# Optimization experiments

Measured on AMD Instinct MI355X. Metric: run time of the kernel, lower is better.

## Reference

```python
import jax, jax.numpy as jnp
import numpy as np

N = 100000   # nodes
E = 1600000  # edges
G = 64       # graphs
D_IN, D_H, D_OUT = 128, 128, 64


def setup_inputs() -> dict:
    key = jax.random.key(0)
    ks = jax.random.split(key, 24)
    def p(k, shape, fan_in):
        return jax.random.normal(k, shape, jnp.float32) / np.sqrt(fan_in)
    inp = {
        "x": jax.random.normal(ks[0], (N, D_IN), jnp.float32),
        "W0r": p(ks[1], (D_H, D_IN), D_IN), "W0i": p(ks[2], (D_H, D_IN), D_IN),
        "b0r": jnp.zeros((D_H,), jnp.float32), "b0i": jnp.zeros((D_H,), jnp.float32),
        "M0r": p(ks[3], (D_H, D_H), D_H), "M0i": p(ks[4], (D_H, D_H), D_H),
        "c0r": jnp.zeros((D_H,), jnp.float32), "c0i": jnp.zeros((D_H,), jnp.float32),
        "t0r": jnp.float32(1.0), "t0i": jnp.zeros((1,), jnp.float32),
        "W1r": p(ks[5], (D_OUT, D_H), D_H), "W1i": p(ks[6], (D_OUT, D_H), D_H),
        "b1r": jnp.zeros((D_OUT,), jnp.float32), "b1i": jnp.zeros((D_OUT,), jnp.float32),
        "M1r": p(ks[7], (D_OUT, D_OUT), D_OUT), "M1i": p(ks[8], (D_OUT, D_OUT), D_OUT),
        "c1r": jnp.zeros((D_OUT,), jnp.float32), "c1i": jnp.zeros((D_OUT,), jnp.float32),
        "t1r": jnp.float32(1.0), "t1i": jnp.zeros((1,), jnp.float32),
        "edge_index": jax.random.randint(ks[9], (2, E), 0, N, dtype=jnp.int64),
        "batch": jnp.sort(jax.random.randint(ks[10], (N,), 0, G, dtype=jnp.int64)),
    }
    return inp


def _complex_relu(z):
    return jax.nn.relu(z.real) + 1j * jax.nn.relu(z.imag)


def _layer(x, Wr, Wi, br, bi, Mr, Mi, cr, ci, tr, ti, src, dst):
    # complex linear: x @ W^T + b
    W = Wr + 1j * Wi
    x = x @ W.T + (br + 1j * bi)
    x = _complex_relu(x)
    t = tr + 1j * ti  # complex time param, shape [1]
    time_factor = jnp.exp(-1j * t)
    # msg_lin applied at node level (linear commutes with gather), then gather at src
    m = (x @ (Mr + 1j * Mi).T + (cr + 1j * ci)) * time_factor
    aggr = jax.ops.segment_sum(m[src], dst, num_segments=N)
    ef = jnp.exp(-1j * t * 0.5)
    return x * ef + aggr * (1 - ef)


def reference(x, W0r, W0i, b0r, b0i, M0r, M0i, c0r, c0i, t0r, t0i,
              W1r, W1i, b1r, b1i, M1r, M1i, c1r, c1i, t1r, t1i,
              edge_index, batch):
    src, dst = edge_index[0], edge_index[1]
    xc = x.astype(jnp.complex64)
    xc = _layer(xc, W0r, W0i, b0r, b0i, M0r, M0i, c0r, c0i, t0r, t0i, src, dst)
    xc = _layer(xc, W1r, W1i, b1r, b1i, M1r, M1i, c1r, c1i, t1r, t1i, src, dst)
    a = jnp.abs(xc)  # [N, D_OUT] float32
    sums = jax.ops.segment_sum(a, batch, num_segments=G)
    counts = jax.ops.segment_sum(jnp.ones((N,), a.dtype), batch, num_segments=G)
    mean = sums / jnp.clip(counts, 1.0)[:, None]
    return jax.nn.log_softmax(mean, axis=1)
```

## Files before the change

kernel.cpp:

```cpp
#include <hip/hip_runtime.h>

typedef __attribute__((ext_vector_type(8))) short bf16x8;
typedef __attribute__((ext_vector_type(4))) float f32x4;

__device__ __forceinline__ float b2f(unsigned short u) {
    return __uint_as_float(((unsigned int)u) << 16);
}
__device__ __forceinline__ unsigned short f2b(float f) {
    unsigned int u = __float_as_uint(f);
    unsigned int r = (u + 0x7FFFu + ((u >> 16) & 1u)) >> 16;
    return (unsigned short)r;
}

__global__ __launch_bounds__(256) void prep_v_cplx_kernel(
    const float* __restrict__ Wr, const float* __restrict__ Wi,
    unsigned short* __restrict__ V, int J, int K)
{
    int idx = blockIdx.x * 256 + threadIdx.x;
    if (idx >= J * K) return;
    int j = idx / K, kk = idx % K;
    float wr = Wr[idx], wi = Wi[idx];
    int Kr = 2 * K;
    unsigned short* r0 = V + (size_t)(2 * j) * Kr + 2 * kk;
    unsigned short* r1 = V + (size_t)(2 * j + 1) * Kr + 2 * kk;
    r0[0] = f2b(wr);  r0[1] = f2b(-wi);
    r1[0] = f2b(wi);  r1[1] = f2b(wr);
}

__global__ __launch_bounds__(256) void prep_v_real_kernel(
    const float* __restrict__ Wr, const float* __restrict__ Wi,
    unsigned short* __restrict__ V, int J, int K)
{
    int idx = blockIdx.x * 256 + threadIdx.x;
    if (idx >= J * K) return;
    int j = idx / K, k = idx % K;
    V[(size_t)(2 * j) * K + k]     = f2b(Wr[idx]);
    V[(size_t)(2 * j + 1) * K + k] = f2b(Wi[idx]);
}

template<int Kr, int TWOJ, bool REAL_IN, bool CRELU, bool MIX, bool WF8>
__global__ __launch_bounds__(256) void mfma_cgemm_kernel(
    const void* __restrict__ Xv,
    const unsigned short* __restrict__ Vg,
    const float* __restrict__ br, const float* __restrict__ bi,
    const float* __restrict__ trp, const float* __restrict__ tip,
    const unsigned short* __restrict__ Hin, const int* __restrict__ degp,
    unsigned short* __restrict__ Out, unsigned char* __restrict__ Of8,
    int nNodes)
{
    constexpr int TILES  = TWOJ / 16;
    constexpr int FT     = TILES / 4;
    constexpr int CHUNKS = Kr / 32;
    constexpr int VROW   = 40;
    static_assert(TILES % 4 == 0, "TILES % 4");

    __shared__ __align__(16) unsigned short sV[TWOJ * VROW];
    __shared__ __align__(16) unsigned short sA[64 * VROW];

    const int tid  = threadIdx.x;
    const int w    = tid >> 6;
    const int lane = tid & 63;
    const int l15  = lane & 15;
    const int q    = lane >> 4;
    const int n0   = blockIdx.x * 64;
    const int tq   = w * FT;

    f32x4 acc[FT][4];
    #pragma unroll
    for (int t = 0; t < FT; ++t)
        #pragma unroll
        for (int nt = 0; nt < 4; ++nt) acc[t][nt] = (f32x4){0.f, 0.f, 0.f, 0.f};

    for (int kc = 0; kc < CHUNKS; ++kc) {
        #pragma unroll
        for (int it = 0; it < TWOJ / 64; ++it) {
            int idx = it * 256 + tid;
            int row = idx >> 2;
            int seg = idx & 3;
            *(uint4*)(sV + row * VROW + seg * 8) =
                *(const uint4*)(Vg + (size_t)row * Kr + kc * 32 + seg * 8);
        }
        if constexpr (REAL_IN) {
            const float* X = (const float*)Xv;
            #pragma unroll
            for (int it = 0; it < 2; ++it) {
                int idx = it * 256 + tid;
                int nl = idx >> 3;
                int cg = idx & 7;
                int n  = n0 + nl;
                float4 v = make_float4(0.f, 0.f, 0.f, 0.f);
                if (n < nNodes)
                    v = *(const float4*)(X + (size_t)n * Kr + kc * 32 + cg * 4);
                *(ushort4*)(sA + nl * VROW + cg * 4) =
                    make_ushort4(f2b(v.x), f2b(v.y), f2b(v.z), f2b(v.w));
            }
        } else {
            const unsigned short* X = (const unsigned short*)Xv;
            int nl  = tid >> 2;
            int seg = tid & 3;
            int n   = n0 + nl;
            uint4 v = make_uint4(0, 0, 0, 0);
            if (n < nNodes)
                v = *(const uint4*)(X + (size_t)n * Kr + kc * 32 + seg * 8);
            *(uint4*)(sA + nl * VROW + seg * 8) = v;
        }
        __syncthreads();

        bf16x8 bfrag[4];
        #pragma unroll
        for (int nt = 0; nt < 4; ++nt)
            bfrag[nt] = *(const bf16x8*)(sA + (nt * 16 + l15) * VROW + q * 8);
        #pragma unroll
        for (int t = 0; t < FT; ++t) {
            bf16x8 afrag = *(const bf16x8*)(sV + ((tq + t) * 16 + l15) * VROW + q * 8);
            #pragma unroll
            for (int nt = 0; nt < 4; ++nt)
                acc[t][nt] = __builtin_amdgcn_mfma_f32_16x16x32_bf16(
                    afrag, bfrag[nt], acc[t][nt], 0, 0, 0);
        }
        __syncthreads();
    }

    float Fr = 1.f, Fi = 0.f, efr = 1.f, efi = 0.f;
    if constexpr (MIX) {
        float tr = trp[0], ti = tip[0];
        float er  = expf(ti);
        float tfr =  er * cosf(tr);
        float tfi = -er * sinf(tr);
        float eh  = expf(0.5f * ti);
        efr =  eh * cosf(0.5f * tr);
        efi = -eh * sinf(0.5f * tr);
        float omr = 1.f - efr, omi = -efi;
        Fr = tfr * omr - tfi * omi;
        Fi = tfr * omi + tfi * omr;
    }
    #pragma unroll
    for (int nt = 0; nt < 4; ++nt) {
        int n = n0 + nt * 16 + l15;
        if (n >= nNodes) continue;
        float dg = 0.f;
        if constexpr (MIX) dg = (float)degp[n];
        #pragma unroll
        for (int t = 0; t < FT; ++t) {
            int f0 = (tq + t) * 16 + q * 4;
            int j0 = f0 >> 1;
            float re0, im0, re1, im1;
            if constexpr (MIX) {
                float ar0 = acc[t][nt][0] + dg * br[j0];
                float ai0 = acc[t][nt][1] + dg * bi[j0];
                float ar1 = acc[t][nt][2] + dg * br[j0 + 1];
                float ai1 = acc[t][nt][3] + dg * bi[j0 + 1];
                re0 = ar0 * Fr - ai0 * Fi;  im0 = ar0 * Fi + ai0 * Fr;
                re1 = ar1 * Fr - ai1 * Fi;  im1 = ar1 * Fi + ai1 * Fr;
                ushort4 hu = *(const ushort4*)(Hin + (size_t)n * TWOJ + f0);
                float hr0 = b2f(hu.x), hi0 = b2f(hu.y), hr1 = b2f(hu.z), hi1 = b2f(hu.w);
                re0 += hr0 * efr - hi0 * efi;  im0 += hr0 * efi + hi0 * efr;
                re1 += hr1 * efr - hi1 * efi;  im1 += hr1 * efi + hi1 * efr;
            } else {
                re0 = acc[t][nt][0] + br[j0];
                im0 = acc[t][nt][1] + bi[j0];
                re1 = acc[t][nt][2] + br[j0 + 1];
                im1 = acc[t][nt][3] + bi[j0 + 1];
                if constexpr (CRELU) {
                    re0 = fmaxf(re0, 0.f); im0 = fmaxf(im0, 0.f);
                    re1 = fmaxf(re1, 0.f); im1 = fmaxf(im1, 0.f);
                }
            }
            *(ushort4*)(Out + (size_t)n * TWOJ + f0) =
                make_ushort4(f2b(re0), f2b(im0), f2b(re1), f2b(im1));
            if constexpr (WF8) {
                int pk = 0;
                pk = __builtin_amdgcn_cvt_pk_fp8_f32(re0, im0, pk, false);
                pk = __builtin_amdgcn_cvt_pk_fp8_f32(re1, im1, pk, true);
                *(int*)(Of8 + (size_t)n * TWOJ + f0) = pk;
            }
        }
    }
}

#define EDGE_CHUNK 2048

__global__ __launch_bounds__(256) void build_kernel(
    const int* __restrict__ src, const int* __restrict__ dst,
    int* __restrict__ deg, int* __restrict__ csr, int E, int N)
{
    int x  = blockIdx.x & 7;
    int c  = blockIdx.x >> 3;
    int lo = (int)((long long)N * x / 8);
    int hi = (int)((long long)N * (x + 1) / 8);
    int base = c * EDGE_CHUNK;
    int end  = min(base + EDGE_CHUNK, E);
    for (int e = base + threadIdx.x; e < end; e += 256) {
        int d = __builtin_nontemporal_load(dst + e);
        if (d >= lo && d < hi) {
            int s = __builtin_nontemporal_load(src + e);
            if ((unsigned)s < (unsigned)N) {
                int pos = atomicAdd(&deg[d], 1);
                if (pos < 64) csr[((size_t)d << 6) + pos] = s;
            }
        }
    }
}

template<int ROWE>
__global__ __launch_bounds__(256) void gather_f8_kernel(
    const unsigned char* __restrict__ h8, unsigned short* __restrict__ agg,
    const int* __restrict__ deg, const int* __restrict__ csr, int N)
{
    constexpr int LPR = ROWE / 16;
    constexpr int NPW = 64 / LPR;
    const int tid  = threadIdx.x;
    const int lane = tid & 63;
    const int wid  = (blockIdx.x * 256 + tid) >> 6;
    if (wid * NPW >= N) return;
    const int g    = lane / LPR;
    const int sub  = lane % LPR;
    const int nid  = wid * NPW + g;
    const bool nv  = nid < N;
    int dg = 0;
    if (nv) dg = min(deg[nid], 64);

    uint4 cq0 = make_uint4(0, 0, 0, 0), cq1 = make_uint4(0, 0, 0, 0);
    if (nv) {
        const uint4* cp = (const uint4*)csr + ((size_t)nid << 4);
        cq0 = cp[sub];
        if constexpr (LPR == 8) cq1 = cp[8 + sub];
    }

    int mx = dg;
    mx = max(mx, __shfl_xor(mx, 32, 64));
    mx = max(mx, __shfl_xor(mx, 16, 64));
    if constexpr (LPR == 8) mx = max(mx, __shfl_xor(mx, 8, 64));

    float a[16];
    #pragma unroll
    for (int k = 0; k < 16; ++k) a[k] = 0.f;

    const unsigned char* hp = h8 + sub * 16;
    const int gb = g * LPR;

    #define CVT16(uu)                                                          \
        {                                                                      \
            auto p0 = __builtin_amdgcn_cvt_pk_f32_fp8((uu).x, false);          \
            a[0] += p0[0];   a[1] += p0[1];                                    \
            auto p1 = __builtin_amdgcn_cvt_pk_f32_fp8((uu).x, true);           \
            a[2] += p1[0];   a[3] += p1[1];                                    \
            auto p2 = __builtin_amdgcn_cvt_pk_f32_fp8((uu).y, false);          \
            a[4] += p2[0];   a[5] += p2[1];                                    \
            auto p3 = __builtin_amdgcn_cvt_pk_f32_fp8((uu).y, true);           \
            a[6] += p3[0];   a[7] += p3[1];                                    \
            auto p4 = __builtin_amdgcn_cvt_pk_f32_fp8((uu).z, false);          \
            a[8] += p4[0];   a[9] += p4[1];                                    \
            auto p5 = __builtin_amdgcn_cvt_pk_f32_fp8((uu).z, true);           \
            a[10] += p5[0];  a[11] += p5[1];                                   \
            auto p6 = __builtin_amdgcn_cvt_pk_f32_fp8((uu).w, false);          \
            a[12] += p6[0];  a[13] += p6[1];                                   \
            auto p7 = __builtin_amdgcn_cvt_pk_f32_fp8((uu).w, true);           \
            a[14] += p7[0];  a[15] += p7[1];                                   \
        }

    for (int e = 0; e < mx; e += 8) {
        uint4 cq = cq0;
        if constexpr (LPR == 8) { if (e & 32) cq = cq1; }
        const int o0 = gb + ((e & (4 * LPR - 1)) >> 2);
        const int o1 = o0 + 1;
        int s0 = __shfl((int)cq.x, o0, 64);
        int s1 = __shfl((int)cq.y, o0, 64);
        int s2 = __shfl((int)cq.z, o0, 64);
        int s3 = __shfl((int)cq.w, o0, 64);
        int s4 = __shfl((int)cq.x, o1, 64);
        int s5 = __shfl((int)cq.y, o1, 64);
        int s6 = __shfl((int)cq.z, o1, 64);
        int s7 = __shfl((int)cq.w, o1, 64);
        uint4 u0 = make_uint4(0,0,0,0), u1 = make_uint4(0,0,0,0);
        uint4 u2 = make_uint4(0,0,0,0), u3 = make_uint4(0,0,0,0);
        uint4 u4 = make_uint4(0,0,0,0), u5 = make_uint4(0,0,0,0);
        uint4 u6 = make_uint4(0,0,0,0), u7 = make_uint4(0,0,0,0);
        if (e + 0 < dg) u0 = *(const uint4*)(hp + (size_t)(unsigned)s0 * ROWE);
        if (e + 1 < dg) u1 = *(const uint4*)(hp + (size_t)(unsigned)s1 * ROWE);
        if (e + 2 < dg) u2 = *(const uint4*)(hp + (size_t)(unsigned)s2 * ROWE);
        if (e + 3 < dg) u3 = *(const uint4*)(hp + (size_t)(unsigned)s3 * ROWE);
        if (e + 4 < dg) u4 = *(const uint4*)(hp + (size_t)(unsigned)s4 * ROWE);
        if (e + 5 < dg) u5 = *(const uint4*)(hp + (size_t)(unsigned)s5 * ROWE);
        if (e + 6 < dg) u6 = *(const uint4*)(hp + (size_t)(unsigned)s6 * ROWE);
        if (e + 7 < dg) u7 = *(const uint4*)(hp + (size_t)(unsigned)s7 * ROWE);
        CVT16(u0) CVT16(u1) CVT16(u2) CVT16(u3)
        CVT16(u4) CVT16(u5) CVT16(u6) CVT16(u7)
    }
    #undef CVT16

    if (nv) {
        unsigned short* op = agg + (size_t)nid * ROWE + sub * 16;
        *(ushort4*)(op)      = make_ushort4(f2b(a[0]),  f2b(a[1]),  f2b(a[2]),  f2b(a[3]));
        *(ushort4*)(op + 4)  = make_ushort4(f2b(a[4]),  f2b(a[5]),  f2b(a[6]),  f2b(a[7]));
        *(ushort4*)(op + 8)  = make_ushort4(f2b(a[8]),  f2b(a[9]),  f2b(a[10]), f2b(a[11]));
        *(ushort4*)(op + 12) = make_ushort4(f2b(a[12]), f2b(a[13]), f2b(a[14]), f2b(a[15]));
    }
}

__global__ __launch_bounds__(256) void abs_reduce_kernel(
    const unsigned short* __restrict__ z, const int* __restrict__ batch,
    float* __restrict__ sums, int N)
{
    constexpr int NPW = 16;
    int wid  = (blockIdx.x * 256 + threadIdx.x) >> 6;
    int lane = threadIdx.x & 63;
    int nBeg = wid * NPW;
    if (nBeg >= N) return;
    int nEnd = min(nBeg + NPW, N);

    float acc = 0.f;
    int cur_g = batch[nBeg];
    for (int n = nBeg; n < nEnd; ++n) {
        unsigned int u = *(const unsigned int*)(z + ((size_t)n << 7) + (lane << 1));
        float zr = b2f((unsigned short)(u & 0xffffu));
        float zi = b2f((unsigned short)(u >> 16));
        float a = sqrtf(zr * zr + zi * zi);
        int g = batch[n];
        if (g != cur_g) {
            if ((unsigned)cur_g < 64u) unsafeAtomicAdd(&sums[cur_g * 64 + lane], acc);
            acc = 0.f;
            cur_g = g;
        }
        acc += a;
    }
    if ((unsigned)cur_g < 64u) unsafeAtomicAdd(&sums[cur_g * 64 + lane], acc);
}

__global__ __launch_bounds__(64) void finalize_kernel(
    const float* __restrict__ sums, const int* __restrict__ batch,
    float* __restrict__ out, int N)
{
    int g = blockIdx.x, d = threadIdx.x;
    __shared__ int cnt_s;
    if (d == 0) {
        int lo = 0, hi = N;
        while (lo < hi) { int mid = (lo + hi) >> 1; if (batch[mid] < g) lo = mid + 1; else hi = mid; }
        int lo2 = lo, hi2 = N;
        while (lo2 < hi2) { int mid = (lo2 + hi2) >> 1; if (batch[mid] < g + 1) lo2 = mid + 1; else hi2 = mid; }
        cnt_s = lo2 - lo;
    }
    __syncthreads();
    float c = fmaxf((float)cnt_s, 1.0f);
    float m = sums[g * 64 + d] / c;
    float mx = m;
    #pragma unroll
    for (int o = 32; o > 0; o >>= 1) mx = fmaxf(mx, __shfl_xor(mx, o, 64));
    float e = expf(m - mx);
    float s = e;
    #pragma unroll
    for (int o = 32; o > 0; o >>= 1) s += __shfl_xor(s, o, 64);
    out[g * 64 + d] = m - mx - logf(s);
}

extern "C" void kernel_launch(void* const* d_in, const int* in_sizes, int n_in,
                              void* d_out, int out_size, void* d_ws, size_t ws_size,
                              hipStream_t stream)
{
    const float* x   = (const float*)d_in[0];
    const float* W0r = (const float*)d_in[1];
    const float* W0i = (const float*)d_in[2];
    const float* b0r = (const float*)d_in[3];
    const float* b0i = (const float*)d_in[4];
    const float* M0r = (const float*)d_in[5];
    const float* M0i = (const float*)d_in[6];
    const float* c0r = (const float*)d_in[7];
    const float* c0i = (const float*)d_in[8];
    const float* t0r = (const float*)d_in[9];
    const float* t0i = (const float*)d_in[10];
    const float* W1r = (const float*)d_in[11];
    const float* W1i = (const float*)d_in[12];
    const float* b1r = (const float*)d_in[13];
    const float* b1i = (const float*)d_in[14];
    const float* M1r = (const float*)d_in[15];
    const float* M1i = (const float*)d_in[16];
    const float* c1r = (const float*)d_in[17];
    const float* c1i = (const float*)d_in[18];
    const float* t1r = (const float*)d_in[19];
    const float* t1i = (const float*)d_in[20];
    const int* edge  = (const int*)d_in[21];
    const int* batch = (const int*)d_in[22];

    const int N = in_sizes[0] / 128;
    const int E = in_sizes[21] / 2;
    const int* src = edge;
    const int* dst = edge + E;

    unsigned short* h0   = (unsigned short*)d_ws;
    unsigned short* aggA = h0 + (size_t)N * 256;
    unsigned short* h1   = aggA + (size_t)N * 256;
    unsigned short* aggB = h1 + (size_t)N * 128;
    int*   deg  = (int*)(aggB + (size_t)N * 128);
    int*   csr  = deg + N;
    float* sums = (float*)(csr + (size_t)N * 64);
    unsigned short* V0  = (unsigned short*)(sums + 4096);
    unsigned short* VM0 = V0  + 256 * 128;
    unsigned short* V1  = VM0 + 256 * 256;
    unsigned short* VM1 = V1  + 128 * 256;
    unsigned char* hf8 = (unsigned char*)(VM1 + 128 * 128);

    const int gemmGrid = (N + 63) / 64;
    const int xcdEdgeGrid = ((E + EDGE_CHUNK - 1) / EDGE_CHUNK) * 8;
    const int g256Grid = (N + 15) / 16;
    const int g128Grid = (N + 31) / 32;
    const int wave16Grid = ((N + 15) / 16 * 64 + 255) / 256;

    hipMemsetAsync(deg, 0, N * sizeof(int), stream);
    hipMemsetAsync(sums, 0, 4096 * sizeof(float), stream);
    prep_v_real_kernel<<<(128 * 128 + 255) / 256, 256, 0, stream>>>(W0r, W0i, V0, 128, 128);
    prep_v_cplx_kernel<<<(128 * 128 + 255) / 256, 256, 0, stream>>>(M0r, M0i, VM0, 128, 128);
    prep_v_cplx_kernel<<<(64 * 128 + 255) / 256, 256, 0, stream>>>(W1r, W1i, V1, 64, 128);
    prep_v_cplx_kernel<<<(64 * 64 + 255) / 256, 256, 0, stream>>>(M1r, M1i, VM1, 64, 64);
    build_kernel<<<xcdEdgeGrid, 256, 0, stream>>>(src, dst, deg, csr, E, N);

    mfma_cgemm_kernel<128,256,true,true,false,true><<<gemmGrid, 256, 0, stream>>>(
        x, V0, b0r, b0i, nullptr, nullptr, nullptr, nullptr, h0, hf8, N);
    gather_f8_kernel<256><<<g256Grid, 256, 0, stream>>>(hf8, aggA, deg, csr, N);
    mfma_cgemm_kernel<256,256,false,false,true,false><<<gemmGrid, 256, 0, stream>>>(
        aggA, VM0, c0r, c0i, t0r, t0i, h0, deg, h0, nullptr, N);

    mfma_cgemm_kernel<256,128,false,true,false,true><<<gemmGrid, 256, 0, stream>>>(
        h0, V1, b1r, b1i, nullptr, nullptr, nullptr, nullptr, h1, hf8, N);
    gather_f8_kernel<128><<<g128Grid, 256, 0, stream>>>(hf8, aggB, deg, csr, N);
    mfma_cgemm_kernel<128,128,false,false,true,false><<<gemmGrid, 256, 0, stream>>>(
        aggB, VM1, c1r, c1i, t1r, t1i, h1, deg, h1, nullptr, N);

    abs_reduce_kernel<<<wave16Grid, 256, 0, stream>>>(h1, batch, sums, N);
    finalize_kernel<<<64, 64, 0, stream>>>(sums, batch, (float*)d_out, N);
}
```

Before: 501.1 us.

## Merge prep kernels and memsets, co-schedule CSR build with first GEMM

Replaces the two memsets and four weight-prep launches with a single prep kernel that also zeroes the degree and sums buffers. The edge-bucketing CSR build now runs as extra blocks appended to the first-layer GEMM grid, so the atomic scatter can overlap with MFMA work instead of running as a separate serial launch. The fp32 input read in the first GEMM switches to nontemporal loads. This cuts launch overhead and idle gaps, but the fused grid mixes memory-bound atomic blocks with compute blocks, which may compete for bandwidth.

Result: slower. 529.4 us (+5.6%).

```diff
diff --git a/kernel.cpp b/kernel.cpp
--- a/kernel.cpp
+++ b/kernel.cpp
@@ -12,33 +12,53 @@
     return (unsigned short)r;
 }
 
-__global__ __launch_bounds__(256) void prep_v_cplx_kernel(
-    const float* __restrict__ Wr, const float* __restrict__ Wi,
-    unsigned short* __restrict__ V, int J, int K)
-{
-    int idx = blockIdx.x * 256 + threadIdx.x;
-    if (idx >= J * K) return;
-    int j = idx / K, kk = idx % K;
-    float wr = Wr[idx], wi = Wi[idx];
-    int Kr = 2 * K;
-    unsigned short* r0 = V + (size_t)(2 * j) * Kr + 2 * kk;
-    unsigned short* r1 = V + (size_t)(2 * j + 1) * Kr + 2 * kk;
-    r0[0] = f2b(wr);  r0[1] = f2b(-wi);
-    r1[0] = f2b(wi);  r1[1] = f2b(wr);
-}
-
-__global__ __launch_bounds__(256) void prep_v_real_kernel(
-    const float* __restrict__ Wr, const float* __restrict__ Wi,
-    unsigned short* __restrict__ V, int J, int K)
-{
-    int idx = blockIdx.x * 256 + threadIdx.x;
-    if (idx >= J * K) return;
-    int j = idx / K, k = idx % K;
-    V[(size_t)(2 * j) * K + k]     = f2b(Wr[idx]);
-    V[(size_t)(2 * j + 1) * K + k] = f2b(Wi[idx]);
-}
-
-template<int Kr, int TWOJ, bool REAL_IN, bool CRELU, bool MIX, bool WF8>
+#define EDGE_CHUNK 2048
+
+__global__ __launch_bounds__(256) void prep_all_kernel(
+    const float* __restrict__ W0r, const float* __restrict__ W0i, unsigned short* __restrict__ V0,
+    const float* __restrict__ M0r, const float* __restrict__ M0i, unsigned short* __restrict__ VM0,
+    const float* __restrict__ W1r, const float* __restrict__ W1i, unsigned short* __restrict__ V1,
+    const float* __restrict__ M1r, const float* __restrict__ M1i, unsigned short* __restrict__ VM1,
+    int* __restrict__ deg, float* __restrict__ sums, int N)
+{
+    int b = blockIdx.x;
+    if (b < 64) {
+        int idx = b * 256 + threadIdx.x;
+        int j = idx >> 7, k = idx & 127;
+        V0[(size_t)(2 * j) * 128 + k]     = f2b(W0r[idx]);
+        V0[(size_t)(2 * j + 1) * 128 + k] = f2b(W0i[idx]);
+    } else if (b < 128) {
+        int idx = (b - 64) * 256 + threadIdx.x;
+        int j = idx >> 7, kk = idx & 127;
+        float wr = M0r[idx], wi = M0i[idx];
+        unsigned short* r0 = VM0 + (size_t)(2 * j) * 256 + 2 * kk;
+        unsigned short* r1 = VM0 + (size_t)(2 * j + 1) * 256 + 2 * kk;
+        r0[0] = f2b(wr);  r0[1] = f2b(-wi);
+        r1[0] = f2b(wi);  r1[1] = f2b(wr);
+    } else if (b < 160) {
+        int idx = (b - 128) * 256 + threadIdx.x;
+        int j = idx >> 7, kk = idx & 127;
+        float wr = W1r[idx], wi = W1i[idx];
+        unsigned short* r0 = V1 + (size_t)(2 * j) * 256 + 2 * kk;
+        unsigned short* r1 = V1 + (size_t)(2 * j + 1) * 256 + 2 * kk;
+        r0[0] = f2b(wr);  r0[1] = f2b(-wi);
+        r1[0] = f2b(wi);  r1[1] = f2b(wr);
+    } else if (b < 176) {
+        int idx = (b - 160) * 256 + threadIdx.x;
+        int j = idx >> 6, kk = idx & 63;
+        float wr = M1r[idx], wi = M1i[idx];
+        unsigned short* r0 = VM1 + (size_t)(2 * j) * 128 + 2 * kk;
+        unsigned short* r1 = VM1 + (size_t)(2 * j + 1) * 128 + 2 * kk;
+        r0[0] = f2b(wr);  r0[1] = f2b(-wi);
+        r1[0] = f2b(wi);  r1[1] = f2b(wr);
+    } else {
+        int idx = (b - 176) * 256 + threadIdx.x;
+        if (idx < N) deg[idx] = 0;
+        else if (idx - N < 4096) sums[idx - N] = 0.f;
+    }
+}
+
+template<int Kr, int TWOJ, bool REAL_IN, bool CRELU, bool MIX, bool WF8, bool BUILD>
 __global__ __launch_bounds__(256) void mfma_cgemm_kernel(
     const void* __restrict__ Xv,
     const unsigned short* __restrict__ Vg,
@@ -46,6 +66,8 @@
     const float* __restrict__ trp, const float* __restrict__ tip,
     const unsigned short* __restrict__ Hin, const int* __restrict__ degp,
     unsigned short* __restrict__ Out, unsigned char* __restrict__ Of8,
+    const int* __restrict__ esrc, const int* __restrict__ edst,
+    int* __restrict__ degw, int* __restrict__ csrw, int E, int nGemm,
     int nNodes)
 {
     constexpr int TILES  = TWOJ / 16;
@@ -56,6 +78,29 @@
 
     __shared__ __align__(16) unsigned short sV[TWOJ * VROW];
     __shared__ __align__(16) unsigned short sA[64 * VROW];
+
+    if constexpr (BUILD) {
+        if (blockIdx.x >= nGemm) {
+            int vb = blockIdx.x - nGemm;
+            int x  = vb & 7;
+            int c  = vb >> 3;
+            int lo = (int)((long long)nNodes * x / 8);
+            int hi = (int)((long long)nNodes * (x + 1) / 8);
+            int base = c * EDGE_CHUNK;
+            int end  = min(base + EDGE_CHUNK, E);
+            for (int e = base + threadIdx.x; e < end; e += 256) {
+                int d = __builtin_nontemporal_load(edst + e);
+                if (d >= lo && d < hi) {
+                    int s = __builtin_nontemporal_load(esrc + e);
+                    if ((unsigned)s < (unsigned)nNodes) {
+                        int pos = atomicAdd(&degw[d], 1);
+                        if (pos < 64) csrw[((size_t)d << 6) + pos] = s;
+                    }
+                }
+            }
+            return;
+        }
+    }
 
     const int tid  = threadIdx.x;
     const int w    = tid >> 6;
@@ -88,11 +133,12 @@
                 int nl = idx >> 3;
                 int cg = idx & 7;
                 int n  = n0 + nl;
-                float4 v = make_float4(0.f, 0.f, 0.f, 0.f);
+                f32x4 v = (f32x4){0.f, 0.f, 0.f, 0.f};
                 if (n < nNodes)
-                    v = *(const float4*)(X + (size_t)n * Kr + kc * 32 + cg * 4);
+                    v = __builtin_nontemporal_load(
+                        (const f32x4*)(X + (size_t)n * Kr + kc * 32 + cg * 4));
                 *(ushort4*)(sA + nl * VROW + cg * 4) =
-                    make_ushort4(f2b(v.x), f2b(v.y), f2b(v.z), f2b(v.w));
+                    make_ushort4(f2b(v[0]), f2b(v[1]), f2b(v[2]), f2b(v[3]));
             }
         } else {
             const unsigned short* X = (const unsigned short*)Xv;
@@ -178,30 +224,6 @@
     }
 }
 
-#define EDGE_CHUNK 2048
-
-__global__ __launch_bounds__(256) void build_kernel(
-    const int* __restrict__ src, const int* __restrict__ dst,
-    int* __restrict__ deg, int* __restrict__ csr, int E, int N)
-{
-    int x  = blockIdx.x & 7;
-    int c  = blockIdx.x >> 3;
-    int lo = (int)((long long)N * x / 8);
-    int hi = (int)((long long)N * (x + 1) / 8);
-    int base = c * EDGE_CHUNK;
-    int end  = min(base + EDGE_CHUNK, E);
-    for (int e = base + threadIdx.x; e < end; e += 256) {
-        int d = __builtin_nontemporal_load(dst + e);
-        if (d >= lo && d < hi) {
-            int s = __builtin_nontemporal_load(src + e);
-            if ((unsigned)s < (unsigned)N) {
-                int pos = atomicAdd(&deg[d], 1);
-                if (pos < 64) csr[((size_t)d << 6) + pos] = s;
-            }
-        }
-    }
-}
-
 template<int ROWE>
 __global__ __launch_bounds__(256) void gather_f8_kernel(
     const unsigned char* __restrict__ h8, unsigned short* __restrict__ agg,
@@ -399,31 +421,32 @@
     unsigned short* VM1 = V1  + 128 * 256;
     unsigned char* hf8 = (unsigned char*)(VM1 + 128 * 128);
 
-    const int gemmGrid = (N + 63) / 64;
-    const int xcdEdgeGrid = ((E + EDGE_CHUNK - 1) / EDGE_CHUNK) * 8;
-    const int g256Grid = (N + 15) / 16;
-    const int g128Grid = (N + 31) / 32;
+    const int gemmGrid  = (N + 63) / 64;
+    const int buildGrid = ((E + EDGE_CHUNK - 1) / EDGE_CHUNK) * 8;
+    const int fusedGrid = gemmGrid + buildGrid;
+    const int prepGrid  = 176 + (N + 4096 + 255) / 256;
+    const int g256Grid  = (N + 15) / 16;
+    const int g128Grid  = (N + 31) / 32;
     const int wave16Grid = ((N + 15) / 16 * 64 + 255) / 256;
 
-    hipMemsetAsync(deg, 0, N * sizeof(int), stream);
-    hipMemsetAsync(sums, 0, 4096 * sizeof(float), stream);
-    prep_v_real_kernel<<<(128 * 128 + 255) / 256, 256, 0, stream>>>(W0r, W0i, V0, 128, 128);
-    prep_v_cplx_kernel<<<(128 * 128 + 255) / 256, 256, 0, stream>>>(M0r, M0i, VM0, 128, 128);
-    prep_v_cplx_kernel<<<(64 * 128 + 255) / 256, 256, 0, stream>>>(W1r, W1i, V1, 64, 128);
-    prep_v_cplx_kernel<<<(64 * 64 + 255) / 256, 256, 0, stream>>>(M1r, M1i, VM1, 64, 64);
-    build_kernel<<<xcdEdgeGrid, 256, 0, stream>>>(src, dst, deg, csr, E, N);
-
-    mfma_cgemm_kernel<128,256,true,true,false,true><<<gemmGrid, 256, 0, stream>>>(
-        x, V0, b0r, b0i, nullptr, nullptr, nullptr, nullptr, h0, hf8, N);
+    prep_all_kernel<<<prepGrid, 256, 0, stream>>>(
+        W0r, W0i, V0, M0r, M0i, VM0, W1r, W1i, V1, M1r, M1i, VM1, deg, sums, N);
+
+    mfma_cgemm_kernel<128,256,true,true,false,true,true><<<fusedGrid, 256, 0, stream>>>(
+        x, V0, b0r, b0i, nullptr, nullptr, nullptr, nullptr, h0, hf8,
+        src, dst, deg, csr, E, gemmGrid, N);
     gather_f8_kernel<256><<<g256Grid, 256, 0, stream>>>(hf8, aggA, deg, csr, N);
-    mfma_cgemm_kernel<256,256,false,false,true,false><<<gemmGrid, 256, 0, stream>>>(
-        aggA, VM0, c0r, c0i, t0r, t0i, h0, deg, h0, nullptr, N);
-
-    mfma_cgemm_kernel<256,128,false,true,false,true><<<gemmGrid, 256, 0, stream>>>(
-        h0, V1, b1r, b1i, nullptr, nullptr, nullptr, nullptr, h1, hf8, N);
+    mfma_cgemm_kernel<256,256,false,false,true,false,false><<<gemmGrid, 256, 0, stream>>>(
+        aggA, VM0, c0r, c0i, t0r, t0i, h0, deg, h0, nullptr,
+        nullptr, nullptr, nullptr, nullptr, 0, gemmGrid, N);
+
+    mfma_cgemm_kernel<256,128,false,true,false,true,false><<<gemmGrid, 256, 0, stream>>>(
+        h0, V1, b1r, b1i, nullptr, nullptr, nullptr, nullptr, h1, hf8,
+        nullptr, nullptr, nullptr, nullptr, 0, gemmGrid, N);
     gather_f8_kernel<128><<<g128Grid, 256, 0, stream>>>(hf8, aggB, deg, csr, N);
-    mfma_cgemm_kernel<128,128,false,false,true,false><<<gemmGrid, 256, 0, stream>>>(
-        aggB, VM1, c1r, c1i, t1r, t1i, h1, deg, h1, nullptr, N);
+    mfma_cgemm_kernel<128,128,false,false,true,false,false><<<gemmGrid, 256, 0, stream>>>(
+        aggB, VM1, c1r, c1i, t1r, t1i, h1, deg, h1, nullptr,
+        nullptr, nullptr, nullptr, nullptr, 0, gemmGrid, N);
 
     abs_reduce_kernel<<<wave16Grid, 256, 0, stream>>>(h1, batch, sums, N);
     finalize_kernel<<<64, 64, 0, stream>>>(sums, batch, (float*)d_out, N);
```
